# Kernel tuning notes

Hardware: AMD Instinct MI355X
Metric: run time of the kernel (lower is better)

## Reference

```python
import jax, jax.numpy as jnp
import numpy as np
import math

D_MODEL = 1024
N_HEADS = 16
HEAD_DIM = D_MODEL // N_HEADS
N_LEVELS = 4
B = 8
MAX_LEN = 1024
LN_EPS = 1e-5


def setup_inputs() -> dict:
    key = jax.random.key(0)
    ks = jax.random.split(key, 6)
    lengths = np.array([1024, 768, 512, 896, 640, 1024, 576, 704], dtype=np.int32)
    N = int(lengths.sum())  # 6144
    batch_offsets = jnp.asarray(np.concatenate([[0], np.cumsum(lengths)]).astype(np.int32))
    x = jax.random.normal(ks[0], (N, D_MODEL), jnp.float32)
    levels = jax.random.randint(ks[1], (N, 1), 0, N_LEVELS).astype(jnp.float32)
    coords = jax.random.uniform(ks[2], (N, 2), jnp.float32) * 64.0
    positions = jnp.concatenate([levels, coords], axis=-1)  # [N, 3] = (level, y, x)
    ln_gamma = jnp.ones((D_MODEL,), jnp.float32)
    ln_beta = jnp.zeros((D_MODEL,), jnp.float32)
    w_qkv = jax.random.normal(ks[3], (D_MODEL, 3 * D_MODEL), jnp.float32) / math.sqrt(D_MODEL)
    w_out = jax.random.normal(ks[4], (D_MODEL, D_MODEL), jnp.float32) / math.sqrt(D_MODEL)
    # learned per-level, per-head rotary frequencies for 2 spatial coords
    base = 10.0 ** (-2.0 * np.arange(HEAD_DIM // 2) / HEAD_DIM)  # rope_theta = 10.0
    rope_freqs = (jnp.asarray(base, jnp.float32)[None, None, :, None]
                  * (1.0 + 0.1 * jax.random.normal(ks[5], (N_LEVELS, N_HEADS, HEAD_DIM // 2, 2), jnp.float32)))
    return {"x": x, "positions": positions, "batch_offsets": batch_offsets,
            "ln_gamma": ln_gamma, "ln_beta": ln_beta, "w_qkv": w_qkv,
            "w_out": w_out, "rope_freqs": rope_freqs}


def _layernorm(x, g, b):
    mu = jnp.mean(x, axis=-1, keepdims=True)
    var = jnp.mean(jnp.square(x - mu), axis=-1, keepdims=True)
    return (x - mu) * jax.lax.rsqrt(var + LN_EPS) * g + b


def _forward(x, positions, batch_offsets, ln_gamma, ln_beta, w_qkv, w_out, rope_freqs):
    N = x.shape[0]
    residual = x
    h = _layernorm(x, ln_gamma, ln_beta)
    q, k, v = jnp.split(h @ w_qkv, 3, axis=-1)  # each [N, D]

    # ragged -> padded batch layout
    tok = jnp.arange(N)
    batch_ids = jnp.searchsorted(batch_offsets[1:], tok, side='right')  # [N]
    pos_in_seq = tok - batch_offsets[batch_ids]                         # [N]
    lengths = batch_offsets[1:] - batch_offsets[:-1]                    # [B]
    valid = jnp.arange(MAX_LEN)[None, :] < lengths[:, None]             # [B, L]

    def pad(t, fill=0.0):
        out = jnp.full((B, MAX_LEN) + t.shape[1:], fill, t.dtype)
        return out.at[batch_ids, pos_in_seq].set(t)

    qp = pad(q).reshape(B, MAX_LEN, N_HEADS, HEAD_DIM)
    kp = pad(k).reshape(B, MAX_LEN, N_HEADS, HEAD_DIM)
    vp = pad(v).reshape(B, MAX_LEN, N_HEADS, HEAD_DIM)
    posp = pad(positions, fill=1.0)  # padded positions filled with ones (as in torch code)

    # multilevel RoPE: per-level learned freqs over 2 spatial coords
    lvl = jnp.clip(posp[..., 0].astype(jnp.int32), 0, N_LEVELS - 1)  # [B, L]
    f = rope_freqs[lvl]                                              # [B, L, H, K, 2]
    ang = jnp.einsum('blhkc,blc->blhk', f, posp[..., 1:])            # [B, L, H, K]
    cos, sin = jnp.cos(ang), jnp.sin(ang)

    def rot(t):  # rotate consecutive pairs of head_dim
        t = t.reshape(B, MAX_LEN, N_HEADS, HEAD_DIM // 2, 2)
        a, b = t[..., 0], t[..., 1]
        return jnp.stack([a * cos - b * sin, a * sin + b * cos], axis=-1).reshape(
            B, MAX_LEN, N_HEADS, HEAD_DIM)

    qr, kr = rot(qp), rot(kp)

    # masked SDPA (padded keys excluded; padded query rows are dropped on un-pad)
    scale = 1.0 / math.sqrt(HEAD_DIM)
    scores = jnp.einsum('blhd,bmhd->bhlm', qr, kr) * scale
    scores = jnp.where(valid[:, None, None, :], scores, jnp.float32(-1e9))
    attn = jax.nn.softmax(scores, axis=-1)
    o = jnp.einsum('bhlm,bmhd->blhd', attn, vp).reshape(B, MAX_LEN, D_MODEL)

    o = o[batch_ids, pos_in_seq]  # back to packed [N, D]
    return o @ w_out + residual


def reference(x, positions, batch_offsets, ln_gamma, ln_beta, w_qkv, w_out, rope_freqs):
    return _forward(x, positions, batch_offsets, ln_gamma, ln_beta, w_qkv, w_out, rope_freqs)
```

## Files before the change

### kernel.cpp

```cpp
#include <hip/hip_runtime.h>


typedef float  f32x4  __attribute__((ext_vector_type(4)));
typedef __bf16 bf16x8 __attribute__((ext_vector_type(8)));
typedef __bf16 bf16x4 __attribute__((ext_vector_type(4)));
typedef short  s16x4  __attribute__((ext_vector_type(4)));
typedef short  s16x8  __attribute__((ext_vector_type(8)));
typedef unsigned short u16x4 __attribute__((ext_vector_type(4)));

typedef __attribute__((address_space(1))) void as1_void_t;
typedef __attribute__((address_space(3))) void as3_void_t;

static __device__ __forceinline__ unsigned short f2bf(float f) {
  unsigned int u = __float_as_uint(f);
  u += 0x7fffu + ((u >> 16) & 1u);
  return (unsigned short)(u >> 16);
}
static __device__ __forceinline__ float bf2f(unsigned short s) {
  return __uint_as_float(((unsigned int)s) << 16);
}

static __device__ __forceinline__ void gload_lds16(const void* g, void* l) {
  __builtin_amdgcn_global_load_lds((as1_void_t*)g, (as3_void_t*)l, 16, 0, 0);
}

static __device__ __forceinline__ f32x4 mfma32(bf16x8 a, bf16x8 b, f32x4 c) {
  return __builtin_amdgcn_mfma_f32_16x16x32_bf16(a, b, c, 0, 0, 0);
}
static __device__ __forceinline__ f32x4 mfma16(s16x4 a, s16x4 b, f32x4 c) {
  return __builtin_amdgcn_mfma_f32_16x16x16bf16_1k(a, b, c, 0, 0, 0);
}

__global__ __launch_bounds__(256) void ln_kernel(
    const float* __restrict__ x, const float* __restrict__ gamma,
    const float* __restrict__ beta, unsigned short* __restrict__ h, int Ntok) {
  int row  = blockIdx.x * 4 + (threadIdx.x >> 6);
  int lane = threadIdx.x & 63;
  const float* xr = x + (size_t)row * 1024;
  f32x4 v[4];
  float s = 0.f, ss = 0.f;
#pragma unroll
  for (int c = 0; c < 4; ++c) {
    v[c] = *(const f32x4*)(xr + c * 256 + lane * 4);
#pragma unroll
    for (int j = 0; j < 4; ++j) { s += v[c][j]; ss += v[c][j] * v[c][j]; }
  }
#pragma unroll
  for (int d = 1; d < 64; d <<= 1) {
    s  += __shfl_xor(s, d);
    ss += __shfl_xor(ss, d);
  }
  float mu  = s * (1.f / 1024.f);
  float var = ss * (1.f / 1024.f) - mu * mu;
  float inv = rsqrtf(var + 1e-5f);
#pragma unroll
  for (int c = 0; c < 4; ++c) {
    f32x4 gv = *(const f32x4*)(gamma + c * 256 + lane * 4);
    f32x4 bv = *(const f32x4*)(beta  + c * 256 + lane * 4);
    u16x4 hv;
#pragma unroll
    for (int j = 0; j < 4; ++j) hv[j] = f2bf((v[c][j] - mu) * inv * gv[j] + bv[j]);
    *(u16x4*)(h + (size_t)row * 1024 + c * 256 + lane * 4) = hv;
  }
}

__global__ __launch_bounds__(256) void transpose_bf16(
    const float* __restrict__ in, unsigned short* __restrict__ out, int R, int C) {
  __shared__ unsigned short tile[64][65];
  int c0 = blockIdx.x * 64, r0 = blockIdx.y * 64;
  int t = threadIdx.x;
  int tr = t >> 6, tc = t & 63;
#pragma unroll
  for (int i = 0; i < 16; ++i) {
    int rr = i * 4 + tr;
    tile[tc][rr] = f2bf(in[(size_t)(r0 + rr) * C + c0 + tc]);
  }
  __syncthreads();
#pragma unroll
  for (int i = 0; i < 16; ++i) {
    int cc = i * 4 + tr;
    out[(size_t)(c0 + cc) * R + r0 + tc] = tile[cc][tc];
  }
}

__global__ __launch_bounds__(256) void gemm_qkv(
    const unsigned short* __restrict__ A, const unsigned short* __restrict__ Bt,
    unsigned short* __restrict__ Cqkv, int M, int K) {
  __shared__ unsigned short Alds[128 * 32];
  __shared__ unsigned short Blds[128 * 32];
  int n0 = blockIdx.x * 128, m0 = blockIdx.y * 128;
  int t = threadIdx.x, lane = t & 63, wave = t >> 6;
  int wr = wave >> 1, wc = wave & 1;
  int r = lane & 15, g = lane >> 4;
  f32x4 acc[4][4] = {};

  int srow = lane >> 2;
  int scol = (lane & 3) * 8;

  for (int k0 = 0; k0 < K; k0 += 32) {
    __syncthreads();
#pragma unroll
    for (int c = 0; c < 2; ++c) {
      int seg = wave * 2 + c;
      gload_lds16(A  + (size_t)(m0 + seg * 16 + srow) * K + k0 + scol,
                  Alds + seg * 16 * 32);
      gload_lds16(Bt + (size_t)(n0 + seg * 16 + srow) * K + k0 + scol,
                  Blds + seg * 16 * 32);
    }
    __syncthreads();
    bf16x8 a[4], b[4];
#pragma unroll
    for (int m = 0; m < 4; ++m)
      a[m] = *(const bf16x8*)(Alds + (wr * 64 + m * 16 + r) * 32 + g * 8);
#pragma unroll
    for (int n = 0; n < 4; ++n)
      b[n] = *(const bf16x8*)(Blds + (wc * 64 + n * 16 + r) * 32 + g * 8);
#pragma unroll
    for (int m = 0; m < 4; ++m)
#pragma unroll
      for (int n = 0; n < 4; ++n)
        acc[m][n] = mfma32(a[m], b[n], acc[m][n]);
  }

#pragma unroll
  for (int mi = 0; mi < 4; ++mi) {
    int grow0 = m0 + wr * 64 + mi * 16 + g * 4;
#pragma unroll
    for (int ni = 0; ni < 4; ++ni) {
      int gcol = n0 + wc * 64 + ni * 16 + r;
      f32x4 v = acc[mi][ni];
#pragma unroll
      for (int e = 0; e < 4; ++e) {
        int which = gcol >> 10, rem = gcol & 1023, hh = rem >> 6, d = rem & 63;
        Cqkv[((size_t)(which * 16 + hh) * M + grow0 + e) * 64 + d] = f2bf(v[e]);
      }
    }
  }
}

__global__ __launch_bounds__(256) void gemm_out(
    const unsigned short* __restrict__ A, const unsigned short* __restrict__ Bt,
    const float* __restrict__ residual, float* __restrict__ Cf,
    int M, int Ncols, int K) {
  __shared__ unsigned short Alds[128 * 32];
  __shared__ unsigned short Blds[128 * 32];
  int n0 = blockIdx.x * 128, m0 = blockIdx.y * 128;
  int t = threadIdx.x, lane = t & 63, wave = t >> 6;
  int wr = wave >> 1, wc = wave & 1;
  int r = lane & 15, g = lane >> 4;
  f32x4 acc[4][4] = {};

  int srow = lane >> 2;
  int scol = (lane & 3) * 8;

  for (int k0 = 0; k0 < K; k0 += 32) {
    __syncthreads();
#pragma unroll
    for (int c = 0; c < 2; ++c) {
      int seg = wave * 2 + c;
      gload_lds16(A  + (size_t)(m0 + seg * 16 + srow) * K + k0 + scol,
                  Alds + seg * 16 * 32);
      gload_lds16(Bt + (size_t)(n0 + seg * 16 + srow) * K + k0 + scol,
                  Blds + seg * 16 * 32);
    }
    __syncthreads();
    bf16x8 a[4], b[4];
#pragma unroll
    for (int m = 0; m < 4; ++m)
      a[m] = *(const bf16x8*)(Alds + (wr * 64 + m * 16 + r) * 32 + g * 8);
#pragma unroll
    for (int n = 0; n < 4; ++n)
      b[n] = *(const bf16x8*)(Blds + (wc * 64 + n * 16 + r) * 32 + g * 8);
#pragma unroll
    for (int m = 0; m < 4; ++m)
#pragma unroll
      for (int n = 0; n < 4; ++n)
        acc[m][n] = mfma32(a[m], b[n], acc[m][n]);
  }

#pragma unroll
  for (int mi = 0; mi < 4; ++mi) {
    int grow0 = m0 + wr * 64 + mi * 16 + g * 4;
#pragma unroll
    for (int ni = 0; ni < 4; ++ni) {
      int gcol = n0 + wc * 64 + ni * 16 + r;
      f32x4 v = acc[mi][ni];
#pragma unroll
      for (int e = 0; e < 4; ++e)
        Cf[(size_t)(grow0 + e) * Ncols + gcol] =
            v[e] + residual[(size_t)(grow0 + e) * Ncols + gcol];
    }
  }
}

__global__ __launch_bounds__(256) void rope_kernel(
    unsigned short* __restrict__ QKV, const float* __restrict__ pos,
    const float* __restrict__ freqs, int Ntok) {
  int t = blockIdx.x * 256 + threadIdx.x;
  if (t >= Ntok * 512) return;
  int kk = t & 31, h = (t >> 5) & 15, i = t >> 9;
  float lvlf = pos[i * 3 + 0];
  float py   = pos[i * 3 + 1];
  float px   = pos[i * 3 + 2];
  int lvl = (int)lvlf;
  lvl = lvl < 0 ? 0 : (lvl > 3 ? 3 : lvl);
  const float* fp = freqs + (((lvl * 16 + h) * 32 + kk) << 1);
  float ang = fp[0] * py + fp[1] * px;
  float s, c;
  __sincosf(ang, &s, &c);
  size_t qoff = ((size_t)h * Ntok + i) * 64 + 2 * kk;
  size_t koff = qoff + (size_t)16 * Ntok * 64;
  unsigned int q2 = *(const unsigned int*)(QKV + qoff);
  float qa = bf2f((unsigned short)(q2 & 0xffff));
  float qb = bf2f((unsigned short)(q2 >> 16));
  *(unsigned int*)(QKV + qoff) =
      (unsigned int)f2bf(qa * c - qb * s) | ((unsigned int)f2bf(qa * s + qb * c) << 16);
  unsigned int k2 = *(const unsigned int*)(QKV + koff);
  float ka = bf2f((unsigned short)(k2 & 0xffff));
  float kb = bf2f((unsigned short)(k2 >> 16));
  *(unsigned int*)(QKV + koff) =
      (unsigned int)f2bf(ka * c - kb * s) | ((unsigned int)f2bf(ka * s + kb * c) << 16);
}

__global__ __launch_bounds__(256) void vtrans_kernel(
    const unsigned short* __restrict__ Vp, unsigned short* __restrict__ VtG,
    int Ntok) {
  __shared__ unsigned short tile[64][72];
  int blk = blockIdx.x;
  int h = blk & 15, t0 = (blk >> 4) * 64;
  int t = threadIdx.x;
  {
    int tok = t >> 2, dc = (t & 3) * 16;
    const unsigned short* src = Vp + ((size_t)h * Ntok + t0 + tok) * 64 + dc;
    *(s16x8*)&tile[tok][dc]     = *(const s16x8*)src;
    *(s16x8*)&tile[tok][dc + 8] = *(const s16x8*)(src + 8);
  }
  __syncthreads();
  {
    int d = t >> 2, tc = (t & 3) * 16;
    s16x8 o0, o1;
#pragma unroll
    for (int j = 0; j < 8; ++j) {
      o0[j] = (short)tile[tc + j][d];
      o1[j] = (short)tile[tc + 8 + j][d];
    }
    unsigned short* dst = VtG + (size_t)(h * 64 + d) * Ntok + t0 + tc;
    *(s16x8*)dst       = o0;
    *(s16x8*)(dst + 8) = o1;
  }
}

__global__ __launch_bounds__(256, 4) void attn_kernel(
    const unsigned short* __restrict__ QKV,
    const unsigned short* __restrict__ VtG, const int* __restrict__ boff,
    unsigned short* __restrict__ O, int Ntok) {
  __shared__ unsigned short Klds[64][72];
  __shared__ unsigned short Vt[64][72];
  const float SCALE_LOG2 = 0.125f * 1.44269504088896340736f;
  const s16x4 ones16 = {(short)0x3F80, (short)0x3F80, (short)0x3F80, (short)0x3F80};

  int bid = blockIdx.x;
  int x = bid & 7, i = bid >> 3;
  int qblk = i & 15;
  int p = x + 8 * (i >> 4);
  int h = p & 15, b = p >> 4;
  int off = boff[b], len = boff[b + 1] - off;
  int q0 = qblk * 64;
  if (q0 >= len) return;
  int t = threadIdx.x, lane = t & 63, wave = t >> 6;
  int r = lane & 15, g4 = lane >> 4;
  const unsigned short* Qg = QKV + (size_t)h * Ntok * 64;
  const unsigned short* Kg = QKV + (size_t)(16 + h) * Ntok * 64;
  int qmax = off + len - 1;

  bf16x8 qf[2];
  {
    int qtok = off + q0 + wave * 16 + r;
    if (qtok > qmax) qtok = qmax;
#pragma unroll
    for (int c = 0; c < 2; ++c)
      qf[c] = *(const bf16x8*)(Qg + (size_t)qtok * 64 + c * 32 + g4 * 8);
  }

  float m = -1e30f;
  f32x4 o[4] = {};
  f32x4 o_sum = {};

  int srow = t >> 2, sseg = t & 3;
  const unsigned short* Vrow = VtG + (size_t)(h * 64 + srow) * Ntok;

  s16x8 kr[2], vr[2];
  {
    int ktok = off + srow; if (ktok > qmax) ktok = qmax;
#pragma unroll
    for (int c = 0; c < 2; ++c)
      kr[c] = *(const s16x8*)(Kg + (size_t)ktok * 64 + sseg * 16 + c * 8);
#pragma unroll
    for (int c = 0; c < 2; ++c) {
      int tc = sseg * 16 + c * 8; if (tc + 8 > len) tc = len - 8;
      vr[c] = *(const s16x8*)(Vrow + off + tc);
    }
  }

  for (int kt = 0; kt < len; kt += 64) {
    asm volatile("s_waitcnt lgkmcnt(0)" ::: "memory");
    __builtin_amdgcn_s_barrier();
    __builtin_amdgcn_sched_barrier(0);
#pragma unroll
    for (int c = 0; c < 2; ++c) {
      *(s16x8*)&Klds[srow][sseg * 16 + c * 8] = kr[c];
      *(s16x8*)&Vt[srow][sseg * 16 + c * 8]   = vr[c];
    }
    int ktn = kt + 64;
    if (ktn < len) {
      int ktok = off + ktn + srow; if (ktok > qmax) ktok = qmax;
#pragma unroll
      for (int c = 0; c < 2; ++c)
        kr[c] = *(const s16x8*)(Kg + (size_t)ktok * 64 + sseg * 16 + c * 8);
#pragma unroll
      for (int c = 0; c < 2; ++c) {
        int tc = ktn + sseg * 16 + c * 8; if (tc + 8 > len) tc = len - 8;
        vr[c] = *(const s16x8*)(Vrow + off + tc);
      }
    }
    asm volatile("s_waitcnt lgkmcnt(0)" ::: "memory");
    __builtin_amdgcn_s_barrier();
    __builtin_amdgcn_sched_barrier(0);

    f32x4 s[4];
    __builtin_amdgcn_s_setprio(1);
#pragma unroll
    for (int sub = 0; sub < 4; ++sub) {
      bf16x8 ka0 = *(const bf16x8*)(&Klds[sub * 16 + r][g4 * 8]);
      bf16x8 ka1 = *(const bf16x8*)(&Klds[sub * 16 + r][32 + g4 * 8]);
      f32x4 acc = {};
      acc = mfma32(ka0, qf[0], acc);
      acc = mfma32(ka1, qf[1], acc);
      s[sub] = acc;
    }
    __builtin_amdgcn_s_setprio(0);

    bool tail = (kt + 64 > len);
    s16x4 pf[4];
    {
      float sc[4][4];
      float ms[4];
#pragma unroll
      for (int sub = 0; sub < 4; ++sub) {
#pragma unroll
        for (int e = 0; e < 4; ++e) {
          float v = s[sub][e];
          if (tail && (kt + sub * 16 + 4 * g4 + e >= len)) v = -1e30f;
          sc[sub][e] = v;
        }
        ms[sub] = fmaxf(fmaxf(sc[sub][0], sc[sub][1]),
                        fmaxf(sc[sub][2], sc[sub][3]));
      }
      float tmax = fmaxf(fmaxf(ms[0], ms[1]), fmaxf(ms[2], ms[3]));
      if (!__all(tmax * SCALE_LOG2 <= m + 8.f)) {
        float tm = tmax * SCALE_LOG2;
        tm = fmaxf(tm, __shfl_xor(tm, 16));
        tm = fmaxf(tm, __shfl_xor(tm, 32));
        float mnew = fmaxf(m, tm);
        float alpha = exp2f(m - mnew);
        m = mnew;
#pragma unroll
        for (int e = 0; e < 4; ++e) o_sum[e] *= alpha;
#pragma unroll
        for (int dt = 0; dt < 4; ++dt)
#pragma unroll
          for (int e = 0; e < 4; ++e) o[dt][e] *= alpha;
      }
#pragma unroll
      for (int sub = 0; sub < 4; ++sub) {
        bf16x4 pb;
#pragma unroll
        for (int e = 0; e < 4; ++e)
          pb[e] = (__bf16)exp2f(fmaf(sc[sub][e], SCALE_LOG2, -m));
        pf[sub] = __builtin_bit_cast(s16x4, pb);
      }
    }

    __builtin_amdgcn_s_setprio(1);
#pragma unroll
    for (int sub = 0; sub < 4; ++sub)
      o_sum = mfma16(pf[sub], ones16, o_sum);
#pragma unroll
    for (int dt = 0; dt < 4; ++dt)
#pragma unroll
      for (int sub = 0; sub < 4; ++sub) {
        s16x4 vf = *(const s16x4*)(&Vt[dt * 16 + r][sub * 16 + 4 * g4]);
        o[dt] = mfma16(pf[sub], vf, o[dt]);
      }
    __builtin_amdgcn_s_setprio(0);
  }

  {
    float il[4];
#pragma unroll
    for (int e = 0; e < 4; ++e) il[e] = 1.0f / o_sum[e];
#pragma unroll
    for (int dt = 0; dt < 4; ++dt)
#pragma unroll
      for (int e = 0; e < 4; ++e) {
        int tl = q0 + wave * 16 + 4 * g4 + e;
        if (tl < len)
          O[(size_t)(off + tl) * 1024 + h * 64 + dt * 16 + r] =
              f2bf(o[dt][e] * il[e]);
      }
  }
}

extern "C" void kernel_launch(void* const* d_in, const int* in_sizes, int n_in,
                              void* d_out, int out_size, void* d_ws, size_t ws_size,
                              hipStream_t stream) {
  const float* x     = (const float*)d_in[0];
  const float* pos   = (const float*)d_in[1];
  const int*   boff  = (const int*)d_in[2];
  const float* gamma = (const float*)d_in[3];
  const float* beta  = (const float*)d_in[4];
  const float* wqkv  = (const float*)d_in[5];
  const float* wout  = (const float*)d_in[6];
  const float* freqs = (const float*)d_in[7];
  float* out = (float*)d_out;
  int N  = in_sizes[0] / 1024;
  int Bn = in_sizes[2] - 1;

  char* ws = (char*)d_ws;
  unsigned short* wqkvT = (unsigned short*)ws;
  unsigned short* woutT = (unsigned short*)(ws + (size_t)3072 * 1024 * 2);
  unsigned short* QKV   = (unsigned short*)(ws + (size_t)3072 * 1024 * 2 +
                                            (size_t)1024 * 1024 * 2);
  size_t qkvBytes = (size_t)48 * N * 64 * 2;
  unsigned short* hbuf = (unsigned short*)((char*)QKV + qkvBytes);
  unsigned short* VtG  = hbuf;
  unsigned short* Vp   = QKV + (size_t)32 * N * 64;
  unsigned short* Obuf = Vp;

  ln_kernel<<<N / 4, 256, 0, stream>>>(x, gamma, beta, hbuf, N);
  transpose_bf16<<<dim3(3072 / 64, 1024 / 64), 256, 0, stream>>>(wqkv, wqkvT, 1024, 3072);
  transpose_bf16<<<dim3(1024 / 64, 1024 / 64), 256, 0, stream>>>(wout, woutT, 1024, 1024);
  gemm_qkv<<<dim3(3072 / 128, N / 128), 256, 0, stream>>>(
      hbuf, wqkvT, QKV, N, 1024);
  rope_kernel<<<(N * 512) / 256, 256, 0, stream>>>(QKV, pos, freqs, N);
  vtrans_kernel<<<16 * (N / 64), 256, 0, stream>>>(Vp, VtG, N);
  attn_kernel<<<8 * 16 * 16, 256, 0, stream>>>(QKV, VtG, boff, Obuf, N);
  gemm_out<<<dim3(1024 / 128, N / 128), 256, 0, stream>>>(
      Obuf, woutT, x, out, N, 1024, 1024);
}
```

Baseline: 186.2 us.

## Compact attention grid to valid query blocks and halve output GEMM M-tile

The attention launch now sizes its grid to the actual number of valid 64-token query blocks across all heads, rather than a full 8x16x16 grid where blocks past a sequence's length exit early. Each block decodes its (query block, batch, head) from the per-batch lengths with a small loop. Separately, the output projection GEMM uses 64-row M tiles instead of 128, doubling the block count to improve CU occupancy and load balance. The cost is extra index math per attention block and more B-tile reloads in the output GEMM. The grid size N/64 assumes every sequence length is a multiple of 64.

```diff
diff --git a/kernel.cpp b/kernel.cpp
--- a/kernel.cpp
+++ b/kernel.cpp
@@ -138,49 +138,49 @@
   }
 }
 
-__global__ __launch_bounds__(256) void gemm_out(
+__global__ __launch_bounds__(256) void gemm_out64(
     const unsigned short* __restrict__ A, const unsigned short* __restrict__ Bt,
     const float* __restrict__ residual, float* __restrict__ Cf,
     int M, int Ncols, int K) {
-  __shared__ unsigned short Alds[128 * 32];
+  __shared__ unsigned short Alds[64 * 32];
   __shared__ unsigned short Blds[128 * 32];
-  int n0 = blockIdx.x * 128, m0 = blockIdx.y * 128;
+  int n0 = blockIdx.x * 128, m0 = blockIdx.y * 64;
   int t = threadIdx.x, lane = t & 63, wave = t >> 6;
   int wr = wave >> 1, wc = wave & 1;
   int r = lane & 15, g = lane >> 4;
-  f32x4 acc[4][4] = {};
+  f32x4 acc[2][4] = {};
 
   int srow = lane >> 2;
   int scol = (lane & 3) * 8;
 
   for (int k0 = 0; k0 < K; k0 += 32) {
     __syncthreads();
+    gload_lds16(A + (size_t)(m0 + wave * 16 + srow) * K + k0 + scol,
+                Alds + wave * 16 * 32);
 #pragma unroll
     for (int c = 0; c < 2; ++c) {
       int seg = wave * 2 + c;
-      gload_lds16(A  + (size_t)(m0 + seg * 16 + srow) * K + k0 + scol,
-                  Alds + seg * 16 * 32);
       gload_lds16(Bt + (size_t)(n0 + seg * 16 + srow) * K + k0 + scol,
                   Blds + seg * 16 * 32);
     }
     __syncthreads();
-    bf16x8 a[4], b[4];
-#pragma unroll
-    for (int m = 0; m < 4; ++m)
-      a[m] = *(const bf16x8*)(Alds + (wr * 64 + m * 16 + r) * 32 + g * 8);
+    bf16x8 a[2], b[4];
+#pragma unroll
+    for (int m = 0; m < 2; ++m)
+      a[m] = *(const bf16x8*)(Alds + (wr * 32 + m * 16 + r) * 32 + g * 8);
 #pragma unroll
     for (int n = 0; n < 4; ++n)
       b[n] = *(const bf16x8*)(Blds + (wc * 64 + n * 16 + r) * 32 + g * 8);
 #pragma unroll
-    for (int m = 0; m < 4; ++m)
+    for (int m = 0; m < 2; ++m)
 #pragma unroll
       for (int n = 0; n < 4; ++n)
         acc[m][n] = mfma32(a[m], b[n], acc[m][n]);
   }
 
 #pragma unroll
-  for (int mi = 0; mi < 4; ++mi) {
-    int grow0 = m0 + wr * 64 + mi * 16 + g * 4;
+  for (int mi = 0; mi < 2; ++mi) {
+    int grow0 = m0 + wr * 32 + mi * 16 + g * 4;
 #pragma unroll
     for (int ni = 0; ni < 4; ++ni) {
       int gcol = n0 + wc * 64 + ni * 16 + r;
@@ -260,13 +260,30 @@
   const s16x4 ones16 = {(short)0x3F80, (short)0x3F80, (short)0x3F80, (short)0x3F80};
 
   int bid = blockIdx.x;
-  int x = bid & 7, i = bid >> 3;
-  int qblk = i & 15;
-  int p = x + 8 * (i >> 4);
-  int h = p & 15, b = p >> 4;
+  int x = bid & 7, idx = bid >> 3;
+  int nq[8];
+#pragma unroll
+  for (int bb = 0; bb < 8; ++bb) nq[bb] = (boff[bb + 1] - boff[bb]) >> 6;
+  int j = 0, rem = idx;
+  for (int it = 0; it < 16; ++it) {
+    int c = 0;
+#pragma unroll
+    for (int bb = 0; bb < 8; ++bb) c += (nq[bb] > j) ? 2 : 0;
+    if (rem < c) break;
+    rem -= c; ++j;
+  }
+  int k = 0;
+  {
+    int c2 = 0;
+#pragma unroll
+    for (int kk = 0; kk < 16; ++kk)
+      if (nq[kk >> 1] > j) { if (c2 == rem) k = kk; ++c2; }
+  }
+  int h = (x + 8 * k) & 15, b = k >> 1, qblk = j;
   int off = boff[b], len = boff[b + 1] - off;
   int q0 = qblk * 64;
   if (q0 >= len) return;
+
   int t = threadIdx.x, lane = t & 63, wave = t >> 6;
   int r = lane & 15, g4 = lane >> 4;
   const unsigned short* Qg = QKV + (size_t)h * Ntok * 64;
@@ -444,7 +461,7 @@
       hbuf, wqkvT, QKV, N, 1024);
   rope_kernel<<<(N * 512) / 256, 256, 0, stream>>>(QKV, pos, freqs, N);
   vtrans_kernel<<<16 * (N / 64), 256, 0, stream>>>(Vp, VtG, N);
-  attn_kernel<<<8 * 16 * 16, 256, 0, stream>>>(QKV, VtG, boff, Obuf, N);
-  gemm_out<<<dim3(1024 / 128, N / 128), 256, 0, stream>>>(
+  attn_kernel<<<16 * (N / 64), 256, 0, stream>>>(QKV, VtG, boff, Obuf, N);
+  gemm_out64<<<dim3(1024 / 128, N / 64), 256, 0, stream>>>(
       Obuf, woutT, x, out, N, 1024, 1024);
 }
```

New measurement: 188.8 us. No clear change (+1.4%).
